# Kernel optimization log

Measured on AMD Instinct MI355X. Metric: run time of the kernel, lower is better.

Reference implementation:

```python
import jax, jax.numpy as jnp
import numpy as np

N_SUPPORT = 8192
N_QUERY = 8192
INPUT_DIM = 1024
EMBED_DIM = 512
N_CLASSES = 64


def setup_inputs() -> dict:
    key = jax.random.key(0)
    k1, k2, k3, k4 = jax.random.split(key, 4)
    support_data = jax.random.normal(k1, (N_SUPPORT, INPUT_DIM), dtype=jnp.float32)
    query_data = jax.random.normal(k2, (N_QUERY, INPUT_DIM), dtype=jnp.float32)
    support_labels = jax.random.randint(k3, (N_SUPPORT,), 0, N_CLASSES, dtype=jnp.int32)
    W = jax.random.normal(k4, (INPUT_DIM, EMBED_DIM), dtype=jnp.float32) * (1.0 / np.sqrt(INPUT_DIM))
    return {"support_data": support_data, "support_labels": support_labels,
            "query_data": query_data, "W": W}


def _l2_normalize(x, eps=1e-12):
    # Matches F.normalize(p=2): x / max(||x||, eps)
    n = jnp.linalg.norm(x, axis=-1, keepdims=True)
    return x / jnp.maximum(n, eps)


def reference(support_data, support_labels, query_data, W):
    # encoder: single linear projection
    s_emb = support_data @ W            # [Ns, D]
    q_emb = query_data @ W              # [Nq, D]
    s_norm = _l2_normalize(s_emb)
    q_norm = _l2_normalize(q_emb)
    # cosine similarities for all query/support pairs: [Nq, Ns]
    sims = q_norm @ s_norm.T
    # per-class sum over support samples (torch.unique -> sorted 0..N_CLASSES-1)
    # segment_sum along the support axis: [N_classes, Nq] -> [Nq, N_classes]
    class_scores = jax.ops.segment_sum(sims.T, support_labels, num_segments=N_CLASSES).T
    return jax.nn.softmax(class_scores, axis=-1)
```

## Files before the change

kernel.cpp:

```cpp
#include <hip/hip_runtime.h>
#include <hip/hip_bf16.h>

#define NS 8192
#define NQ 8192
#define NTOT 16384
#define KDIM 1024
#define ED 512
#define NC 64

typedef __attribute__((ext_vector_type(4))) float fx4;
typedef __attribute__((ext_vector_type(8))) short sx8;
typedef __attribute__((ext_vector_type(8))) unsigned short ux8;

__device__ __forceinline__ unsigned short f2bf(float f) {
  union { float f; unsigned u; } v; v.f = f;
  unsigned r = v.u + 0x7fffu + ((v.u >> 16) & 1u);
  return (unsigned short)(r >> 16);
}
__device__ __forceinline__ float bf2f(unsigned short h) {
  union { unsigned u; float f; } v; v.u = ((unsigned)h) << 16;
  return v.f;
}

__global__ __launch_bounds__(256) void k_prep(
    const float* __restrict__ W, unsigned short* __restrict__ Wtp,
    float* __restrict__ rowssq, float* __restrict__ Pacc) {
  int c = blockIdx.x * 256 + threadIdx.x;
  int lane = c & 63;
  int j    = (c >> 6) & 3;
  int s2   = (c >> 8) & 1;
  int kt   = (c >> 9) & 15;
  int n64  = c >> 13;
  int quad = lane >> 4, ml = lane & 15;
  int n  = n64 * 64 + j * 16 + ml;
  int kb = kt * 64 + (s2 * 4 + quad) * 8;
  ux8 o;
#pragma unroll
  for (int e = 0; e < 8; ++e) o[e] = f2bf(W[(size_t)(kb + e) * ED + n]);
  *(ux8*)&Wtp[(size_t)c * 8] = o;
  if (c < NTOT) rowssq[c] = 0.f;
  if (c < NC * ED) Pacc[c] = 0.f;
}

__global__ __launch_bounds__(512, 2) void k_gemm_embed(
    const float* __restrict__ Xs, const float* __restrict__ Xq,
    const unsigned short* __restrict__ Wtp,
    unsigned short* __restrict__ emb, float* __restrict__ rowssq) {
  __shared__ unsigned short Ash[2][2][64 * 8 * 8];

  int m_blk = blockIdx.x;
  const float* Xsrc = (m_blk < 128)
      ? (Xs + (size_t)m_blk * 64 * KDIM)
      : (Xq + (size_t)(m_blk - 128) * 64 * KDIM);

  int t = threadIdx.x;
  int lane = t & 63, w = t >> 6;
  int quad = lane >> 4, ml = lane & 15;

  const unsigned short* Bbase = Wtp + ((size_t)w * 8192 + lane) * 8;

  fx4 acc[4][4];
#pragma unroll
  for (int i = 0; i < 4; ++i)
#pragma unroll
    for (int j = 0; j < 4; ++j) acc[i][j] = fx4{0.f, 0.f, 0.f, 0.f};

  fx4 avA[2][2], avB[2][2];
  sx8 bfA[4][4], bfB[4][4];

  int am = t >> 3, akq = t & 7;

  auto loadA = [&](int kt, fx4 (&av)[2][2]) {
#pragma unroll
    for (int h = 0; h < 2; ++h) {
      const float* g = &Xsrc[(size_t)am * KDIM + kt * 128 + h * 64 + akq * 8];
      av[h][0] = *(const fx4*)g;
      av[h][1] = *(const fx4*)(g + 4);
    }
  };
  auto writeA = [&](const fx4 (&av)[2][2], int bbuf) {
#pragma unroll
    for (int h = 0; h < 2; ++h) {
      ux8 o;
      o[0] = f2bf(av[h][0].x); o[1] = f2bf(av[h][0].y);
      o[2] = f2bf(av[h][0].z); o[3] = f2bf(av[h][0].w);
      o[4] = f2bf(av[h][1].x); o[5] = f2bf(av[h][1].y);
      o[6] = f2bf(av[h][1].z); o[7] = f2bf(av[h][1].w);
      *(ux8*)&Ash[bbuf][h][((am * 8) + (akq ^ (am & 7))) * 8] = o;
    }
  };
  auto loadB = [&](int kt, sx8 (&bf)[4][4]) {
#pragma unroll
    for (int g = 0; g < 4; ++g) {
      int kt64 = 2 * kt + (g >> 1);
      int s2p = g & 1;
#pragma unroll
      for (int j = 0; j < 4; ++j)
        bf[g][j] = *(const sx8*)&Bbase[(size_t)(kt64 * 512 + s2p * 256 + j * 64) * 8];
    }
  };
  auto compute = [&](int b, const sx8 (&bf)[4][4]) {
#pragma unroll
    for (int g = 0; g < 4; ++g) {
      int kq16 = g * 4 + quad;
      int half = kq16 >> 3, oct = kq16 & 7;
      sx8 af[4];
#pragma unroll
      for (int i = 0; i < 4; ++i) {
        int row = i * 16 + ml;
        af[i] = *(const sx8*)&Ash[b][half][(row * 8 + (oct ^ (row & 7))) * 8];
      }
#pragma unroll
      for (int i = 0; i < 4; ++i)
#pragma unroll
        for (int j = 0; j < 4; ++j)
          acc[i][j] = __builtin_amdgcn_mfma_f32_16x16x32_bf16(af[i], bf[g][j], acc[i][j], 0, 0, 0);
    }
  };
  auto sync_step = [&]() {
    __builtin_amdgcn_sched_barrier(0);
    asm volatile("s_waitcnt lgkmcnt(0)" ::: "memory");
    __builtin_amdgcn_s_barrier();
    __builtin_amdgcn_sched_barrier(0);
  };

  loadB(0, bfA);
  loadA(0, avA);
  loadA(1, avB);
  writeA(avA, 0);
  sync_step();

  for (int it = 0; it < 4; ++it) {
    int kt0 = it * 2;
    {
      loadB(kt0 + 1, bfB);
      loadA(kt0 + 2 < 8 ? kt0 + 2 : 7, avA);
      compute(0, bfA);
      writeA(avB, 1);
      sync_step();
    }
    {
      loadB(kt0 + 2 < 8 ? kt0 + 2 : 7, bfA);
      loadA(kt0 + 3 < 8 ? kt0 + 3 : 7, avB);
      compute(1, bfB);
      writeA(avA, 0);
      sync_step();
    }
  }

  int grow = m_blk * 64;
  int gcol = w * 64;
#pragma unroll
  for (int i = 0; i < 4; ++i) {
#pragma unroll
    for (int r = 0; r < 4; ++r) {
      int mrow = grow + i * 16 + quad * 4 + r;
      float p = 0.f;
#pragma unroll
      for (int j = 0; j < 4; ++j) {
        emb[(size_t)mrow * ED + gcol + j * 16 + ml] = f2bf(acc[i][j][r]);
        p += acc[i][j][r] * acc[i][j][r];
      }
#pragma unroll
      for (int off = 1; off < 16; off <<= 1) p += __shfl_xor(p, off, 16);
      if (ml == 0) atomicAdd(&rowssq[mrow], p);
    }
  }
}

__global__ __launch_bounds__(256) void k_proto(
    const unsigned short* __restrict__ embS, const float* __restrict__ rowssq,
    const int* __restrict__ labels, float* __restrict__ Pacc) {
  __shared__ float Pl[NC * 64];
  int t = threadIdx.x;
#pragma unroll
  for (int i = 0; i < 16; ++i) Pl[i * 256 + t] = 0.f;
  __syncthreads();

  int w = t >> 6, lane = t & 63;
  int ds = blockIdx.y;
  int row0 = blockIdx.x * 256;
#pragma unroll 4
  for (int r = w; r < 256; r += 4) {
    int row = row0 + r;
    int lbl = labels[row];
    float scale = 1.0f / fmaxf(sqrtf(rowssq[row]), 1e-12f);
    float v = bf2f(embS[(size_t)row * ED + ds * 64 + lane]) * scale;
    atomicAdd(&Pl[lbl * 64 + lane], v);
  }
  __syncthreads();

#pragma unroll
  for (int i = 0; i < 16; ++i) {
    int idx = i * 256 + t;
    atomicAdd(&Pacc[(size_t)(idx >> 6) * ED + ds * 64 + (idx & 63)], Pl[idx]);
  }
}

__global__ __launch_bounds__(256) void k_scores(
    const unsigned short* __restrict__ embQ, const float* __restrict__ ssqQ,
    const float* __restrict__ Pacc, float* __restrict__ out) {
  __shared__ unsigned short Pl[4096 * 8];
  int t = threadIdx.x;
#pragma unroll
  for (int i = 0; i < 16; ++i) {
    int c = t + 256 * i;
    int cls = c & 63, ks = c >> 6;
    const float* p = &Pacc[(size_t)cls * ED + ks * 8];
    fx4 p0 = *(const fx4*)p;
    fx4 p1 = *(const fx4*)(p + 4);
    ux8 bb;
    bb[0] = f2bf(p0.x); bb[1] = f2bf(p0.y); bb[2] = f2bf(p0.z); bb[3] = f2bf(p0.w);
    bb[4] = f2bf(p1.x); bb[5] = f2bf(p1.y); bb[6] = f2bf(p1.z); bb[7] = f2bf(p1.w);
    *(ux8*)&Pl[(size_t)c * 8] = bb;
  }
  __syncthreads();

  int w = t >> 6, lane = t & 63;
  int quad = lane >> 4, ml = lane & 15;
  int qrow0 = blockIdx.x * 64 + w * 16;

  fx4 acc[4];
#pragma unroll
  for (int i = 0; i < 4; ++i) acc[i] = fx4{0.f, 0.f, 0.f, 0.f};

#pragma unroll 4
  for (int ki = 0; ki < 16; ++ki) {
    sx8 a = *(const sx8*)&embQ[(size_t)(qrow0 + ml) * ED + ki * 32 + quad * 8];
#pragma unroll
    for (int nt = 0; nt < 4; ++nt) {
      sx8 b = *(const sx8*)&Pl[((ki * 4 + quad) * 64 + nt * 16 + ml) * 8];
      acc[nt] = __builtin_amdgcn_mfma_f32_16x16x32_bf16(a, b, acc[nt], 0, 0, 0);
    }
  }

#pragma unroll
  for (int r = 0; r < 4; ++r) {
    int qq = qrow0 + quad * 4 + r;
    float scale = 1.0f / fmaxf(sqrtf(ssqQ[qq]), 1e-12f);
    float s[4];
#pragma unroll
    for (int nt = 0; nt < 4; ++nt) s[nt] = acc[nt][r] * scale;
    float m = fmaxf(fmaxf(s[0], s[1]), fmaxf(s[2], s[3]));
#pragma unroll
    for (int off = 1; off < 16; off <<= 1) m = fmaxf(m, __shfl_xor(m, off, 16));
    float e[4], ssum = 0.f;
#pragma unroll
    for (int nt = 0; nt < 4; ++nt) { e[nt] = __expf(s[nt] - m); ssum += e[nt]; }
#pragma unroll
    for (int off = 1; off < 16; off <<= 1) ssum += __shfl_xor(ssum, off, 16);
    float inv = 1.0f / ssum;
#pragma unroll
    for (int nt = 0; nt < 4; ++nt)
      out[(size_t)qq * NC + nt * 16 + ml] = e[nt] * inv;
  }
}

extern "C" void kernel_launch(void* const* d_in, const int* in_sizes, int n_in,
                              void* d_out, int out_size, void* d_ws, size_t ws_size,
                              hipStream_t stream) {
  const float* Xs     = (const float*)d_in[0];
  const int*   labels = (const int*)d_in[1];
  const float* Xq     = (const float*)d_in[2];
  const float* W      = (const float*)d_in[3];
  float* out = (float*)d_out;

  char* ws = (char*)d_ws;
  size_t off = 0;
  unsigned short* Wtp = (unsigned short*)(ws + off); off += (size_t)ED * KDIM * 2;
  unsigned short* emb = (unsigned short*)(ws + off); off += (size_t)NTOT * ED * 2;
  float* rowssq = (float*)(ws + off); off += (size_t)NTOT * 4;
  float* Pacc   = (float*)(ws + off); off += (size_t)NC * ED * 4;

  k_prep<<<256, 256, 0, stream>>>(W, Wtp, rowssq, Pacc);
  k_gemm_embed<<<256, 512, 0, stream>>>(Xs, Xq, Wtp, emb, rowssq);
  k_proto<<<dim3(32, 8), 256, 0, stream>>>(emb, rowssq, labels, Pacc);
  k_scores<<<NQ / 64, 256, 0, stream>>>(emb + (size_t)NS * ED, rowssq + NS, Pacc, out);
}
```

Measured before the change: 151.8 us.

## Deepen GEMM K-tile to 256 with single A register buffer

Doubles the K step of the embedding GEMM from 128 to 256, so the block runs 4 iterations with one barrier each instead of 8, and doubles the shared-memory A buffer. A is now staged through a single register set instead of two, and B fragments are loaded in halves that overlap the two compute halves. The sched_barrier fences around the barrier are removed, so the compiler may reorder across it. LDS use doubles to 64KB per block, which can hurt occupancy under launch_bounds(512,2). Less A prefetch depth may also expose more global-load latency.

```diff
diff --git a/kernel.cpp b/kernel.cpp
--- a/kernel.cpp
+++ b/kernel.cpp
@@ -46,7 +46,7 @@
     const float* __restrict__ Xs, const float* __restrict__ Xq,
     const unsigned short* __restrict__ Wtp,
     unsigned short* __restrict__ emb, float* __restrict__ rowssq) {
-  __shared__ unsigned short Ash[2][2][64 * 8 * 8];
+  __shared__ unsigned short Ash[2][4][64 * 8 * 8];
 
   int m_blk = blockIdx.x;
   const float* Xsrc = (m_blk < 128)
@@ -65,87 +65,78 @@
 #pragma unroll
     for (int j = 0; j < 4; ++j) acc[i][j] = fx4{0.f, 0.f, 0.f, 0.f};
 
-  fx4 avA[2][2], avB[2][2];
+  fx4 av[4][2];
   sx8 bfA[4][4], bfB[4][4];
 
   int am = t >> 3, akq = t & 7;
 
-  auto loadA = [&](int kt, fx4 (&av)[2][2]) {
-#pragma unroll
-    for (int h = 0; h < 2; ++h) {
-      const float* g = &Xsrc[(size_t)am * KDIM + kt * 128 + h * 64 + akq * 8];
-      av[h][0] = *(const fx4*)g;
-      av[h][1] = *(const fx4*)(g + 4);
-    }
-  };
-  auto writeA = [&](const fx4 (&av)[2][2], int bbuf) {
-#pragma unroll
-    for (int h = 0; h < 2; ++h) {
+  auto loadA = [&](int kt) {
+#pragma unroll
+    for (int q = 0; q < 4; ++q) {
+      const float* g = &Xsrc[(size_t)am * KDIM + kt * 256 + q * 64 + akq * 8];
+      av[q][0] = *(const fx4*)g;
+      av[q][1] = *(const fx4*)(g + 4);
+    }
+  };
+  auto writeA = [&](int bbuf) {
+#pragma unroll
+    for (int q = 0; q < 4; ++q) {
       ux8 o;
-      o[0] = f2bf(av[h][0].x); o[1] = f2bf(av[h][0].y);
-      o[2] = f2bf(av[h][0].z); o[3] = f2bf(av[h][0].w);
-      o[4] = f2bf(av[h][1].x); o[5] = f2bf(av[h][1].y);
-      o[6] = f2bf(av[h][1].z); o[7] = f2bf(av[h][1].w);
-      *(ux8*)&Ash[bbuf][h][((am * 8) + (akq ^ (am & 7))) * 8] = o;
-    }
-  };
-  auto loadB = [&](int kt, sx8 (&bf)[4][4]) {
-#pragma unroll
-    for (int g = 0; g < 4; ++g) {
-      int kt64 = 2 * kt + (g >> 1);
+      o[0] = f2bf(av[q][0].x); o[1] = f2bf(av[q][0].y);
+      o[2] = f2bf(av[q][0].z); o[3] = f2bf(av[q][0].w);
+      o[4] = f2bf(av[q][1].x); o[5] = f2bf(av[q][1].y);
+      o[6] = f2bf(av[q][1].z); o[7] = f2bf(av[q][1].w);
+      *(ux8*)&Ash[bbuf][q][((am * 8) + (akq ^ (am & 7))) * 8] = o;
+    }
+  };
+  auto loadBhalf = [&](int kt, int gbase, sx8 (&bf)[4][4]) {
+#pragma unroll
+    for (int gg = 0; gg < 4; ++gg) {
+      int g = gbase + gg;
+      int kt64 = 4 * kt + (g >> 1);
       int s2p = g & 1;
 #pragma unroll
       for (int j = 0; j < 4; ++j)
-        bf[g][j] = *(const sx8*)&Bbase[(size_t)(kt64 * 512 + s2p * 256 + j * 64) * 8];
-    }
-  };
-  auto compute = [&](int b, const sx8 (&bf)[4][4]) {
-#pragma unroll
-    for (int g = 0; g < 4; ++g) {
-      int kq16 = g * 4 + quad;
-      int half = kq16 >> 3, oct = kq16 & 7;
+        bf[gg][j] = *(const sx8*)&Bbase[(size_t)(kt64 * 512 + s2p * 256 + j * 64) * 8];
+    }
+  };
+  auto computeHalf = [&](int b, int gbase, const sx8 (&bf)[4][4]) {
+#pragma unroll
+    for (int gg = 0; gg < 4; ++gg) {
+      int kq32 = (gbase + gg) * 4 + quad;
+      int qtr = kq32 >> 3, oct = kq32 & 7;
       sx8 af[4];
 #pragma unroll
       for (int i = 0; i < 4; ++i) {
         int row = i * 16 + ml;
-        af[i] = *(const sx8*)&Ash[b][half][(row * 8 + (oct ^ (row & 7))) * 8];
+        af[i] = *(const sx8*)&Ash[b][qtr][(row * 8 + (oct ^ (row & 7))) * 8];
       }
 #pragma unroll
       for (int i = 0; i < 4; ++i)
 #pragma unroll
         for (int j = 0; j < 4; ++j)
-          acc[i][j] = __builtin_amdgcn_mfma_f32_16x16x32_bf16(af[i], bf[g][j], acc[i][j], 0, 0, 0);
+          acc[i][j] = __builtin_amdgcn_mfma_f32_16x16x32_bf16(af[i], bf[gg][j], acc[i][j], 0, 0, 0);
     }
   };
   auto sync_step = [&]() {
-    __builtin_amdgcn_sched_barrier(0);
     asm volatile("s_waitcnt lgkmcnt(0)" ::: "memory");
     __builtin_amdgcn_s_barrier();
-    __builtin_amdgcn_sched_barrier(0);
-  };
-
-  loadB(0, bfA);
-  loadA(0, avA);
-  loadA(1, avB);
-  writeA(avA, 0);
+  };
+
+  loadBhalf(0, 0, bfA);
+  loadA(0);
+  writeA(0);
   sync_step();
 
   for (int it = 0; it < 4; ++it) {
-    int kt0 = it * 2;
-    {
-      loadB(kt0 + 1, bfB);
-      loadA(kt0 + 2 < 8 ? kt0 + 2 : 7, avA);
-      compute(0, bfA);
-      writeA(avB, 1);
-      sync_step();
-    }
-    {
-      loadB(kt0 + 2 < 8 ? kt0 + 2 : 7, bfA);
-      loadA(kt0 + 3 < 8 ? kt0 + 3 : 7, avB);
-      compute(1, bfB);
-      writeA(avA, 0);
-      sync_step();
-    }
+    int b = it & 1;
+    loadBhalf(it, 4, bfB);
+    loadA(it + 1 < 4 ? it + 1 : 3);
+    computeHalf(b, 0, bfA);
+    computeHalf(b, 4, bfB);
+    writeA(b ^ 1);
+    loadBhalf(it + 1 < 4 ? it + 1 : 3, 0, bfA);
+    sync_step();
   }
 
   int grow = m_blk * 64;
```

Result: no change. 153.6 us (+1.2%).
